# Optimization experiments

Hardware: AMD Instinct MI355X
Metric: run time of the kernel (lower is better)

## Reference

```python
import jax, jax.numpy as jnp
import numpy as np

BETA = 1.0
NUM_CLASSES = 64  # upper bound on region ids per image (mask.max()+1 in original)


def setup_inputs() -> dict:
    key = jax.random.key(0)
    k1, k2, k3 = jax.random.split(key, 3)
    B, C, H, W = 16, 3, 512, 512
    inp = jax.random.normal(k1, (B, C, H, W), dtype=jnp.float32)
    tgt = jax.random.normal(k2, (B, C, H, W), dtype=jnp.float32)
    mask = jax.random.randint(k3, (B, H, W), 0, NUM_CLASSES, dtype=jnp.int32)
    return {"input": inp, "target": tgt, "mask": mask}


def reference(input, target, mask):
    B, C, H, W = input.shape
    # per-element L1 (reduce=False)
    loss = jnp.abs(input - target)                      # [B,C,H,W]
    w = jax.lax.stop_gradient(loss)                     # detached copy
    # segmented mean over (channels x region pixels) per (batch, class)
    seg = (jnp.arange(B, dtype=mask.dtype)[:, None, None] * NUM_CLASSES + mask).reshape(-1)  # [B*H*W]
    w_csum = w.sum(axis=1).reshape(-1)                  # sum over channels per pixel, [B*H*W]
    sums = jax.ops.segment_sum(w_csum, seg, num_segments=B * NUM_CLASSES)
    cnts = jax.ops.segment_sum(jnp.ones_like(w_csum), seg, num_segments=B * NUM_CLASSES)
    avg = sums / jnp.maximum(cnts * C, 1.0)             # mean over C*area elements; safe for empty regions
    # broadcast region averages back (same value across channels)
    weight = avg[seg].reshape(B, 1, H, W)               # [B,1,H,W]
    weight = weight / jnp.max(weight)
    weight = jnp.clip(weight, 0.0, 1.0)
    return jnp.mean(loss * (weight * BETA + 1.0))
```

## Files before the change

### kernel.cpp

```cpp
#include <hip/hip_runtime.h>
#include <hip/hip_bf16.h>

#define NUM_CLASSES 64
#define BATCH 16
#define CHAN 3
#define HW (512 * 512)
#define BPB 64
#define THREADS 256
#define NITER 4
#define NREP 4
#define CPAD 8

#define SUM_BITS 23
#define CNT_INC  (1u << SUM_BITS)
#define SUM_MASK32 ((1u << SUM_BITS) - 1u)
#define FIX_SCALE 512.0f
#define INV_FIX (1.0f / 512.0f)

#define CNT_SHIFT 44

__global__ __launch_bounds__(THREADS, 4) void frl_accum(
    const float4* __restrict__ inp,
    const float4* __restrict__ tgt,
    const int4* __restrict__ mask,
    unsigned long long* __restrict__ g_hist)
{
    __shared__ unsigned int s_hist[NREP][NUM_CLASSES + CPAD];
    const int t = threadIdx.x;
    for (int i = t; i < NREP * (NUM_CLASSES + CPAD); i += THREADS)
        ((unsigned int*)s_hist)[i] = 0u;
    __syncthreads();

    const int b   = blockIdx.x / BPB;
    const int blk = blockIdx.x % BPB;
    const int GPB = HW / 4 / BPB;
    const int rep = t & (NREP - 1);

    const int g0    = blk * GPB + t;
    const int cbase = b * (CHAN * HW / 4);
    const int mbase = b * (HW / 4);
    const int CS    = HW / 4;

    int4   m_c;
    float4 i0_c, t0_c, i1_c, t1_c, i2_c, t2_c;
    {
        const int g = g0;
        m_c  = mask[mbase + g];
        i0_c = inp[cbase + 0 * CS + g];
        t0_c = tgt[cbase + 0 * CS + g];
        i1_c = inp[cbase + 1 * CS + g];
        t1_c = tgt[cbase + 1 * CS + g];
        i2_c = inp[cbase + 2 * CS + g];
        t2_c = tgt[cbase + 2 * CS + g];
    }

    #pragma unroll
    for (int it = 0; it < NITER; ++it) {
        int4   m_n;
        float4 i0_n, t0_n, i1_n, t1_n, i2_n, t2_n;
        if (it + 1 < NITER) {
            const int g = g0 + (it + 1) * THREADS;
            m_n  = mask[mbase + g];
            i0_n = inp[cbase + 0 * CS + g];
            t0_n = tgt[cbase + 0 * CS + g];
            i1_n = inp[cbase + 1 * CS + g];
            t1_n = tgt[cbase + 1 * CS + g];
            i2_n = inp[cbase + 2 * CS + g];
            t2_n = tgt[cbase + 2 * CS + g];
        }

        const float l0 = fabsf(i0_c.x - t0_c.x) + fabsf(i1_c.x - t1_c.x) + fabsf(i2_c.x - t2_c.x);
        const float l1 = fabsf(i0_c.y - t0_c.y) + fabsf(i1_c.y - t1_c.y) + fabsf(i2_c.y - t2_c.y);
        const float l2 = fabsf(i0_c.z - t0_c.z) + fabsf(i1_c.z - t1_c.z) + fabsf(i2_c.z - t2_c.z);
        const float l3 = fabsf(i0_c.w - t0_c.w) + fabsf(i1_c.w - t1_c.w) + fabsf(i2_c.w - t2_c.w);

        atomicAdd(&s_hist[rep][m_c.x], CNT_INC + __float2uint_rn(l0 * FIX_SCALE));
        atomicAdd(&s_hist[rep][m_c.y], CNT_INC + __float2uint_rn(l1 * FIX_SCALE));
        atomicAdd(&s_hist[rep][m_c.z], CNT_INC + __float2uint_rn(l2 * FIX_SCALE));
        atomicAdd(&s_hist[rep][m_c.w], CNT_INC + __float2uint_rn(l3 * FIX_SCALE));

        if (it + 1 < NITER) {
            m_c  = m_n;
            i0_c = i0_n; t0_c = t0_n;
            i1_c = i1_n; t1_c = t1_n;
            i2_c = i2_n; t2_c = t2_n;
        }
    }

    __syncthreads();
    if (t < NUM_CLASSES) {
        unsigned int cnt = 0u, sfx = 0u;
        #pragma unroll
        for (int r = 0; r < NREP; ++r) {
            const unsigned int v = s_hist[r][t];
            cnt += v >> SUM_BITS;
            sfx += v & SUM_MASK32;
        }
        atomicAdd(&g_hist[b * NUM_CLASSES + t],
                  ((unsigned long long)cnt << CNT_SHIFT) | (unsigned long long)sfx);
    }
}

__global__ __launch_bounds__(256) void frl_finalize(
    const unsigned long long* __restrict__ g_hist,
    float* __restrict__ out)
{
    const int NSEG = BATCH * NUM_CLASSES;
    __shared__ float s_avg[BATCH * NUM_CLASSES];
    __shared__ float s_sumf[BATCH * NUM_CLASSES];
    __shared__ float red[256];
    const int t = threadIdx.x;
    const unsigned long long SUM_MASK = (1ull << CNT_SHIFT) - 1ull;

    float lmax = 0.0f;
    for (int s = t; s < NSEG; s += 256) {
        const unsigned long long v = g_hist[s];
        const float sum = (float)(v & SUM_MASK) * INV_FIX;
        const float cnt = (float)(v >> CNT_SHIFT);
        const float avg = sum / fmaxf(cnt * (float)CHAN, 1.0f);
        s_sumf[s] = sum;
        s_avg[s] = avg;
        lmax = fmaxf(lmax, avg);
    }
    red[t] = lmax;
    __syncthreads();
    for (int off = 128; off > 0; off >>= 1) {
        if (t < off) red[t] = fmaxf(red[t], red[t + off]);
        __syncthreads();
    }
    const float maxavg = fmaxf(red[0], 1e-30f);
    __syncthreads();

    float part = 0.0f;
    for (int s = t; s < NSEG; s += 256) {
        const float w = fminf(fmaxf(s_avg[s] / maxavg, 0.0f), 1.0f);
        part += s_sumf[s] * (1.0f + w);
    }
    red[t] = part;
    __syncthreads();
    for (int off = 128; off > 0; off >>= 1) {
        if (t < off) red[t] += red[t + off];
        __syncthreads();
    }
    if (t == 0) {
        out[0] = red[0] / (float)((size_t)BATCH * CHAN * HW);
    }
}

extern "C" void kernel_launch(void* const* d_in, const int* in_sizes, int n_in,
                              void* d_out, int out_size, void* d_ws, size_t ws_size,
                              hipStream_t stream) {
    const float4* inp = (const float4*)d_in[0];
    const float4* tgt = (const float4*)d_in[1];
    const int4* mask  = (const int4*)d_in[2];

    unsigned long long* g_hist = (unsigned long long*)d_ws;

    hipMemsetAsync(d_ws, 0, BATCH * NUM_CLASSES * sizeof(unsigned long long), stream);
    frl_accum<<<BATCH * BPB, THREADS, 0, stream>>>(inp, tgt, mask, g_hist);
    frl_finalize<<<1, 256, 0, stream>>>(g_hist, (float*)d_out);
}
```

Before: 139.6 us.

## Split accumulation block into producer and consumer warps with LDS double buffer

Half the threads of each block now load chunks of mask, input and target into a double-buffered shared-memory staging area, while the other half read the previous chunk from LDS, compute the per-pixel L1 sums and do the histogram atomics. The intent is to overlap global loads with the atomic-heavy compute phase, which previously ran in register-prefetch form inside each thread. In exchange, every element makes an extra round trip through LDS, each chunk ends in a block-wide barrier, and only half the threads issue loads or compute at any time. Shared-memory use also grows substantially, which may limit occupancy.

Result: no change. 139.6 us (-0.0%).

```diff
diff --git a/kernel.cpp b/kernel.cpp
--- a/kernel.cpp
+++ b/kernel.cpp
@@ -7,7 +7,9 @@
 #define HW (512 * 512)
 #define BPB 64
 #define THREADS 256
-#define NITER 4
+#define GPB (HW / 4 / BPB)
+#define CHUNK 128
+#define NCHUNK (GPB / CHUNK)
 #define NREP 4
 #define CPAD 8
 
@@ -20,74 +22,101 @@
 #define CNT_SHIFT 44
 
 __global__ __launch_bounds__(THREADS, 4) void frl_accum(
-    const float4* __restrict__ inp,
-    const float4* __restrict__ tgt,
+    const int4* __restrict__ inp,
+    const int4* __restrict__ tgt,
     const int4* __restrict__ mask,
     unsigned long long* __restrict__ g_hist)
 {
+    __shared__ int4 s_buf[2][7][CHUNK];
     __shared__ unsigned int s_hist[NREP][NUM_CLASSES + CPAD];
+
     const int t = threadIdx.x;
     for (int i = t; i < NREP * (NUM_CLASSES + CPAD); i += THREADS)
         ((unsigned int*)s_hist)[i] = 0u;
-    __syncthreads();
 
-    const int b   = blockIdx.x / BPB;
-    const int blk = blockIdx.x % BPB;
-    const int GPB = HW / 4 / BPB;
-    const int rep = t & (NREP - 1);
-
-    const int g0    = blk * GPB + t;
+    const int b     = blockIdx.x / BPB;
+    const int blk   = blockIdx.x % BPB;
     const int cbase = b * (CHAN * HW / 4);
     const int mbase = b * (HW / 4);
     const int CS    = HW / 4;
+    const int gblk  = blk * GPB;
 
-    int4   m_c;
-    float4 i0_c, t0_c, i1_c, t1_c, i2_c, t2_c;
-    {
-        const int g = g0;
-        m_c  = mask[mbase + g];
-        i0_c = inp[cbase + 0 * CS + g];
-        t0_c = tgt[cbase + 0 * CS + g];
-        i1_c = inp[cbase + 1 * CS + g];
-        t1_c = tgt[cbase + 1 * CS + g];
-        i2_c = inp[cbase + 2 * CS + g];
-        t2_c = tgt[cbase + 2 * CS + g];
+    const bool producer = (t < 128);
+    const int  lt = producer ? t : (t - 128);
+
+    __syncthreads();
+
+    if (producer) {
+        const int g = gblk + lt;
+        const int4 r0 = mask[mbase + g];
+        const int4 r1 = inp[cbase + 0 * CS + g];
+        const int4 r2 = tgt[cbase + 0 * CS + g];
+        const int4 r3 = inp[cbase + 1 * CS + g];
+        const int4 r4 = tgt[cbase + 1 * CS + g];
+        const int4 r5 = inp[cbase + 2 * CS + g];
+        const int4 r6 = tgt[cbase + 2 * CS + g];
+        s_buf[0][0][lt] = r0;
+        s_buf[0][1][lt] = r1;
+        s_buf[0][2][lt] = r2;
+        s_buf[0][3][lt] = r3;
+        s_buf[0][4][lt] = r4;
+        s_buf[0][5][lt] = r5;
+        s_buf[0][6][lt] = r6;
+    }
+    __syncthreads();
+
+    #pragma unroll
+    for (int c = 0; c < NCHUNK; ++c) {
+        const int buf = c & 1;
+        if (producer) {
+            if (c + 1 < NCHUNK) {
+                const int g = gblk + (c + 1) * CHUNK + lt;
+                const int4 r0 = mask[mbase + g];
+                const int4 r1 = inp[cbase + 0 * CS + g];
+                const int4 r2 = tgt[cbase + 0 * CS + g];
+                const int4 r3 = inp[cbase + 1 * CS + g];
+                const int4 r4 = tgt[cbase + 1 * CS + g];
+                const int4 r5 = inp[cbase + 2 * CS + g];
+                const int4 r6 = tgt[cbase + 2 * CS + g];
+                s_buf[buf ^ 1][0][lt] = r0;
+                s_buf[buf ^ 1][1][lt] = r1;
+                s_buf[buf ^ 1][2][lt] = r2;
+                s_buf[buf ^ 1][3][lt] = r3;
+                s_buf[buf ^ 1][4][lt] = r4;
+                s_buf[buf ^ 1][5][lt] = r5;
+                s_buf[buf ^ 1][6][lt] = r6;
+            }
+        } else {
+            const int rep = lt & (NREP - 1);
+            const int4 m  = s_buf[buf][0][lt];
+            const int4 a0 = s_buf[buf][1][lt];
+            const int4 b0 = s_buf[buf][2][lt];
+            const int4 a1 = s_buf[buf][3][lt];
+            const int4 b1 = s_buf[buf][4][lt];
+            const int4 a2 = s_buf[buf][5][lt];
+            const int4 b2 = s_buf[buf][6][lt];
+
+            const float l0 = fabsf(__int_as_float(a0.x) - __int_as_float(b0.x))
+                           + fabsf(__int_as_float(a1.x) - __int_as_float(b1.x))
+                           + fabsf(__int_as_float(a2.x) - __int_as_float(b2.x));
+            const float l1 = fabsf(__int_as_float(a0.y) - __int_as_float(b0.y))
+                           + fabsf(__int_as_float(a1.y) - __int_as_float(b1.y))
+                           + fabsf(__int_as_float(a2.y) - __int_as_float(b2.y));
+            const float l2 = fabsf(__int_as_float(a0.z) - __int_as_float(b0.z))
+                           + fabsf(__int_as_float(a1.z) - __int_as_float(b1.z))
+                           + fabsf(__int_as_float(a2.z) - __int_as_float(b2.z));
+            const float l3 = fabsf(__int_as_float(a0.w) - __int_as_float(b0.w))
+                           + fabsf(__int_as_float(a1.w) - __int_as_float(b1.w))
+                           + fabsf(__int_as_float(a2.w) - __int_as_float(b2.w));
+
+            atomicAdd(&s_hist[rep][m.x], CNT_INC + __float2uint_rn(l0 * FIX_SCALE));
+            atomicAdd(&s_hist[rep][m.y], CNT_INC + __float2uint_rn(l1 * FIX_SCALE));
+            atomicAdd(&s_hist[rep][m.z], CNT_INC + __float2uint_rn(l2 * FIX_SCALE));
+            atomicAdd(&s_hist[rep][m.w], CNT_INC + __float2uint_rn(l3 * FIX_SCALE));
+        }
+        __syncthreads();
     }
 
-    #pragma unroll
-    for (int it = 0; it < NITER; ++it) {
-        int4   m_n;
-        float4 i0_n, t0_n, i1_n, t1_n, i2_n, t2_n;
-        if (it + 1 < NITER) {
-            const int g = g0 + (it + 1) * THREADS;
-            m_n  = mask[mbase + g];
-            i0_n = inp[cbase + 0 * CS + g];
-            t0_n = tgt[cbase + 0 * CS + g];
-            i1_n = inp[cbase + 1 * CS + g];
-            t1_n = tgt[cbase + 1 * CS + g];
-            i2_n = inp[cbase + 2 * CS + g];
-            t2_n = tgt[cbase + 2 * CS + g];
-        }
-
-        const float l0 = fabsf(i0_c.x - t0_c.x) + fabsf(i1_c.x - t1_c.x) + fabsf(i2_c.x - t2_c.x);
-        const float l1 = fabsf(i0_c.y - t0_c.y) + fabsf(i1_c.y - t1_c.y) + fabsf(i2_c.y - t2_c.y);
-        const float l2 = fabsf(i0_c.z - t0_c.z) + fabsf(i1_c.z - t1_c.z) + fabsf(i2_c.z - t2_c.z);
-        const float l3 = fabsf(i0_c.w - t0_c.w) + fabsf(i1_c.w - t1_c.w) + fabsf(i2_c.w - t2_c.w);
-
-        atomicAdd(&s_hist[rep][m_c.x], CNT_INC + __float2uint_rn(l0 * FIX_SCALE));
-        atomicAdd(&s_hist[rep][m_c.y], CNT_INC + __float2uint_rn(l1 * FIX_SCALE));
-        atomicAdd(&s_hist[rep][m_c.z], CNT_INC + __float2uint_rn(l2 * FIX_SCALE));
-        atomicAdd(&s_hist[rep][m_c.w], CNT_INC + __float2uint_rn(l3 * FIX_SCALE));
-
-        if (it + 1 < NITER) {
-            m_c  = m_n;
-            i0_c = i0_n; t0_c = t0_n;
-            i1_c = i1_n; t1_c = t1_n;
-            i2_c = i2_n; t2_c = t2_n;
-        }
-    }
-
-    __syncthreads();
     if (t < NUM_CLASSES) {
         unsigned int cnt = 0u, sfx = 0u;
         #pragma unroll
@@ -150,9 +179,9 @@
 extern "C" void kernel_launch(void* const* d_in, const int* in_sizes, int n_in,
                               void* d_out, int out_size, void* d_ws, size_t ws_size,
                               hipStream_t stream) {
-    const float4* inp = (const float4*)d_in[0];
-    const float4* tgt = (const float4*)d_in[1];
-    const int4* mask  = (const int4*)d_in[2];
+    const int4* inp  = (const int4*)d_in[0];
+    const int4* tgt  = (const int4*)d_in[1];
+    const int4* mask = (const int4*)d_in[2];
 
     unsigned long long* g_hist = (unsigned long long*)d_ws;
 
```

## Replace global atomic histogram with per-block partials reduced in finalize

Applied to the files above, without the earlier changes.

Each accumulation block now writes its 64 per-class packed partials to a dedicated slot in workspace, replacing 64-bit global atomics. This removes the memset launch and the atomic contention on the per-batch histogram. The finalize kernel grows to 1024 threads, and each thread sums 64 partials for one (batch, class) before the max and sum reductions. The cost is a serial 64-load reduction per thread in a single-block finalize kernel, plus more workspace memory.

Result: slower. 151.8 us (+8.7%).

```diff
diff --git a/kernel.cpp b/kernel.cpp
--- a/kernel.cpp
+++ b/kernel.cpp
@@ -6,6 +6,7 @@
 #define CHAN 3
 #define HW (512 * 512)
 #define BPB 64
+#define TOTB (BATCH * BPB)
 #define THREADS 256
 #define NITER 4
 #define NREP 4
@@ -23,7 +24,7 @@
     const float4* __restrict__ inp,
     const float4* __restrict__ tgt,
     const int4* __restrict__ mask,
-    unsigned long long* __restrict__ g_hist)
+    unsigned long long* __restrict__ g_part)
 {
     __shared__ unsigned int s_hist[NREP][NUM_CLASSES + CPAD];
     const int t = threadIdx.x;
@@ -96,49 +97,43 @@
             cnt += v >> SUM_BITS;
             sfx += v & SUM_MASK32;
         }
-        atomicAdd(&g_hist[b * NUM_CLASSES + t],
-                  ((unsigned long long)cnt << CNT_SHIFT) | (unsigned long long)sfx);
+        g_part[(size_t)t * TOTB + blockIdx.x] =
+            ((unsigned long long)cnt << CNT_SHIFT) | (unsigned long long)sfx;
     }
 }
 
-__global__ __launch_bounds__(256) void frl_finalize(
-    const unsigned long long* __restrict__ g_hist,
+__global__ __launch_bounds__(1024) void frl_finalize(
+    const unsigned long long* __restrict__ g_part,
     float* __restrict__ out)
 {
-    const int NSEG = BATCH * NUM_CLASSES;
-    __shared__ float s_avg[BATCH * NUM_CLASSES];
-    __shared__ float s_sumf[BATCH * NUM_CLASSES];
-    __shared__ float red[256];
+    __shared__ float red[1024];
     const int t = threadIdx.x;
+    const int c = t & (NUM_CLASSES - 1);
+    const int b = t >> 6;
+
+    const unsigned long long* p = g_part + (size_t)c * TOTB + b * BPB;
+    unsigned long long acc = 0ull;
+    #pragma unroll 8
+    for (int k = 0; k < BPB; ++k) acc += p[k];
+
     const unsigned long long SUM_MASK = (1ull << CNT_SHIFT) - 1ull;
+    const float sum  = (float)(acc & SUM_MASK) * INV_FIX;
+    const float cntf = (float)(acc >> CNT_SHIFT);
+    const float avg  = sum / fmaxf(cntf * (float)CHAN, 1.0f);
 
-    float lmax = 0.0f;
-    for (int s = t; s < NSEG; s += 256) {
-        const unsigned long long v = g_hist[s];
-        const float sum = (float)(v & SUM_MASK) * INV_FIX;
-        const float cnt = (float)(v >> CNT_SHIFT);
-        const float avg = sum / fmaxf(cnt * (float)CHAN, 1.0f);
-        s_sumf[s] = sum;
-        s_avg[s] = avg;
-        lmax = fmaxf(lmax, avg);
-    }
-    red[t] = lmax;
+    red[t] = avg;
     __syncthreads();
-    for (int off = 128; off > 0; off >>= 1) {
+    for (int off = 512; off > 0; off >>= 1) {
         if (t < off) red[t] = fmaxf(red[t], red[t + off]);
         __syncthreads();
     }
     const float maxavg = fmaxf(red[0], 1e-30f);
     __syncthreads();
 
-    float part = 0.0f;
-    for (int s = t; s < NSEG; s += 256) {
-        const float w = fminf(fmaxf(s_avg[s] / maxavg, 0.0f), 1.0f);
-        part += s_sumf[s] * (1.0f + w);
-    }
-    red[t] = part;
+    const float w = fminf(fmaxf(avg / maxavg, 0.0f), 1.0f);
+    red[t] = sum * (1.0f + w);
     __syncthreads();
-    for (int off = 128; off > 0; off >>= 1) {
+    for (int off = 512; off > 0; off >>= 1) {
         if (t < off) red[t] += red[t + off];
         __syncthreads();
     }
@@ -154,9 +149,8 @@
     const float4* tgt = (const float4*)d_in[1];
     const int4* mask  = (const int4*)d_in[2];
 
-    unsigned long long* g_hist = (unsigned long long*)d_ws;
+    unsigned long long* g_part = (unsigned long long*)d_ws;
 
-    hipMemsetAsync(d_ws, 0, BATCH * NUM_CLASSES * sizeof(unsigned long long), stream);
-    frl_accum<<<BATCH * BPB, THREADS, 0, stream>>>(inp, tgt, mask, g_hist);
-    frl_finalize<<<1, 256, 0, stream>>>(g_hist, (float*)d_out);
+    frl_accum<<<TOTB, THREADS, 0, stream>>>(inp, tgt, mask, g_part);
+    frl_finalize<<<1, 1024, 0, stream>>>(g_part, (float*)d_out);
 }
```
